# Kernel optimization log

Hardware: AMD Instinct MI355X
Metric: run time of the kernel (lower is better)

The kernel has to match this reference:

```python
import jax, jax.numpy as jnp
import numpy as np

B, S, H, NH, L = 2, 2048, 2048, 16, 512
HD = H // NH  # head_dim = 128


def setup_inputs() -> dict:
    key = jax.random.key(0)
    k1, k2, k3, k4, k5 = jax.random.split(key, 5)
    scale = 0.02  # mimic xavier-scale init
    return {
        "q": jax.random.normal(k1, (B, S, H), dtype=jnp.float32),
        "latent_kv": jax.random.normal(k2, (B, S, L), dtype=jnp.float32),
        "Wq": jax.random.normal(k3, (H, H), dtype=jnp.float32) * scale,
        "Wkv_expand": jax.random.normal(k4, (2 * H, L), dtype=jnp.float32) * scale,
        "Wout": jax.random.normal(k5, (H, H), dtype=jnp.float32) * scale,
    }


def reference(q, latent_kv, Wq, Wkv_expand, Wout):
    b, sq, _ = q.shape
    sk = latent_kv.shape[1]
    # projections (torch Linear: x @ W.T)
    qp = q @ Wq.T                              # [B,Sq,H]
    kv = latent_kv @ Wkv_expand.T              # [B,Sk,2H]
    k, v = jnp.split(kv, 2, axis=-1)           # each [B,Sk,H]
    # split heads -> [B,NH,S,HD]
    qh = qp.reshape(b, sq, NH, HD).transpose(0, 2, 1, 3)
    kh = k.reshape(b, sk, NH, HD).transpose(0, 2, 1, 3)
    vh = v.reshape(b, sk, NH, HD).transpose(0, 2, 1, 3)
    inv_sqrt_d = 1.0 / jnp.sqrt(jnp.float32(HD))
    scores = jnp.einsum("bhqd,bhkd->bhqk", qh, kh) * inv_sqrt_d
    # causal mask (seq_q == seq_k)
    causal = jnp.tril(jnp.ones((sq, sk), dtype=bool))
    scores = jnp.where(causal, scores, jnp.finfo(scores.dtype).min)
    attn = jax.nn.softmax(scores, axis=-1)
    out = jnp.einsum("bhqk,bhkd->bhqd", attn, vh)  # [B,NH,Sq,HD]
    out = out.transpose(0, 2, 1, 3).reshape(b, sq, H)
    return out @ Wout.T
```

## Files before the change

kernel.cpp:

```cpp
#include <hip/hip_runtime.h>

#define SLEN 2048
#define NHEADS 16
#define HDIM 128

typedef __attribute__((ext_vector_type(8))) short bf16x8;
typedef __attribute__((ext_vector_type(4))) float f32x4;
typedef __attribute__((ext_vector_type(16))) float f32x16;

__device__ __forceinline__ unsigned short f2bf(float f) {
  union { float f; unsigned u; } v; v.f = f;
  unsigned r = v.u + 0x7FFFu + ((v.u >> 16) & 1u);
  return (unsigned short)(r >> 16);
}

__device__ __forceinline__ float bf2f(unsigned short h) {
  union { unsigned u; float f; } v; v.u = (unsigned)h << 16;
  return v.f;
}

__device__ __forceinline__ unsigned pkbf(float a, float b) {
  unsigned r;
  asm("v_cvt_pk_bf16_f32 %0, %1, %2" : "=v"(r) : "v"(a), "v"(b));
  return r;
}

__device__ __forceinline__ void gload16(const void* g, void* l) {
  __builtin_amdgcn_global_load_lds(
      (const __attribute__((address_space(1))) unsigned int*)g,
      (__attribute__((address_space(3))) unsigned int*)l, 16, 0, 0);
}

__global__ __launch_bounds__(256) void cvt_all(const float* __restrict__ q,
                                               const float* __restrict__ Wq,
                                               const float* __restrict__ lat,
                                               const float* __restrict__ Wkv,
                                               const float* __restrict__ Wout,
                                               unsigned short* __restrict__ qo,
                                               unsigned short* __restrict__ Wqo,
                                               unsigned short* __restrict__ lato,
                                               unsigned short* __restrict__ Wkvo,
                                               unsigned short* __restrict__ Wouto) {
  const int blk = blockIdx.x;
  const float* in;
  unsigned short* out;
  int base;
  if (blk < 4096)      { in = q;    out = qo;    base = 0; }
  else if (blk < 6144) { in = Wq;   out = Wqo;   base = 4096; }
  else if (blk < 7168) { in = lat;  out = lato;  base = 6144; }
  else if (blk < 8192) { in = Wkv;  out = Wkvo;  base = 7168; }
  else                 { in = Wout; out = Wouto; base = 8192; }
  const int i = (blk - base) * 256 + threadIdx.x;
  const float4* p = reinterpret_cast<const float4*>(in) + (size_t)i * 2;
  float4 a = p[0], b = p[1];
  uint4 o;
  o.x = (unsigned)f2bf(a.x) | ((unsigned)f2bf(a.y) << 16);
  o.y = (unsigned)f2bf(a.z) | ((unsigned)f2bf(a.w) << 16);
  o.z = (unsigned)f2bf(b.x) | ((unsigned)f2bf(b.y) << 16);
  o.w = (unsigned)f2bf(b.z) | ((unsigned)f2bf(b.w) << 16);
  reinterpret_cast<uint4*>(out)[i] = o;
}

template <bool OUT_F32>
__global__ __launch_bounds__(256, 2) void gemm_bt(const unsigned short* __restrict__ A,
                                                  const unsigned short* __restrict__ B,
                                                  void* __restrict__ Cv,
                                                  int M, int N, int K,
                                                  size_t zB, size_t zC, float scale) {
  __shared__ unsigned short As[4][128 * 32];
  __shared__ unsigned short Bs[4][128 * 32];
  const int tid = threadIdx.x;
  const int lane = tid & 63, wid = tid >> 6;
  const int g = lane >> 4, q = lane & 15;
  const int nbx = N >> 7;
  const int cpx = gridDim.x >> 3;
  const int bid = (blockIdx.x & 7) * cpx + (blockIdx.x >> 3);
  const int bx = bid % nbx, by = bid / nbx;
  const int tM = by << 7, tN = bx << 7;
  const int wm = (wid >> 1) * 64, wn = (wid & 1) * 64;
  const size_t zoff = (size_t)blockIdx.z;
  B += zoff * zB;

  const int sr = tid >> 2, sc = tid & 3;
  const int scs = sc ^ (sr & 3);
  const unsigned short* gA0 = A + (size_t)(tM + sr) * K + (scs << 3);
  const unsigned short* gA1 = A + (size_t)(tM + 64 + sr) * K + (scs << 3);
  const unsigned short* gB0 = B + (size_t)(tN + sr) * K + (scs << 3);
  const unsigned short* gB1 = B + (size_t)(tN + 64 + sr) * K + (scs << 3);

  const int nk = K >> 5;
  const int gq = g ^ (q & 3);

  auto STAGE = [&](int slot, int kt) {
    const size_t ko = (size_t)kt << 5;
    unsigned short* ad = &As[slot][0] + tid * 8;
    unsigned short* bd = &Bs[slot][0] + tid * 8;
    gload16(gA0 + ko, ad);
    gload16(gA1 + ko, ad + 2048);
    gload16(gB0 + ko, bd);
    gload16(gB1 + ko, bd + 2048);
  };

  STAGE(0, 0); STAGE(1, 1); STAGE(2, 2);

  f32x4 acc[4][4] = {};

  for (int t = 0; t < nk; ++t) {
    if (t + 2 < nk)      asm volatile("s_waitcnt vmcnt(8)" ::: "memory");
    else if (t + 1 < nk) asm volatile("s_waitcnt vmcnt(4)" ::: "memory");
    else                 asm volatile("s_waitcnt vmcnt(0)" ::: "memory");
    __builtin_amdgcn_s_barrier();
    if (t + 3 < nk) STAGE((t + 3) & 3, t + 3);

    const int s = t & 3;
    bf16x8 af[4], bfr[4];
#pragma unroll
    for (int i = 0; i < 4; ++i)
      af[i] = *(const bf16x8*)&As[s][(wm + i * 16 + q) * 32 + gq * 8];
#pragma unroll
    for (int j = 0; j < 4; ++j)
      bfr[j] = *(const bf16x8*)&Bs[s][(wn + j * 16 + q) * 32 + gq * 8];
    __builtin_amdgcn_s_setprio(1);
#pragma unroll
    for (int i = 0; i < 4; ++i)
#pragma unroll
      for (int j = 0; j < 4; ++j)
        acc[i][j] = __builtin_amdgcn_mfma_f32_16x16x32_bf16(af[i], bfr[j], acc[i][j], 0, 0, 0);
    __builtin_amdgcn_s_setprio(0);
  }

  if constexpr (OUT_F32) {
    float* C = (float*)Cv + zoff * zC;
#pragma unroll
    for (int i = 0; i < 4; ++i)
#pragma unroll
      for (int j = 0; j < 4; ++j)
#pragma unroll
        for (int r = 0; r < 4; ++r)
          C[(size_t)(tM + wm + i * 16 + g * 4 + r) * N + (tN + wn + j * 16 + q)] =
              acc[i][j][r] * scale;
  } else {
    unsigned short* C = (unsigned short*)Cv + zoff * zC;
#pragma unroll
    for (int i = 0; i < 4; ++i)
#pragma unroll
      for (int j = 0; j < 4; ++j)
#pragma unroll
        for (int r = 0; r < 4; ++r)
          C[(size_t)(tM + wm + i * 16 + g * 4 + r) * N + (tN + wn + j * 16 + q)] =
              f2bf(acc[i][j][r] * scale);
  }
}

__global__ __launch_bounds__(256, 3) void mla_attn(const unsigned short* __restrict__ Q,
                                                   const unsigned short* __restrict__ K,
                                                   const unsigned short* __restrict__ VT,
                                                   unsigned short* __restrict__ Op0,
                                                   unsigned short* __restrict__ Op1,
                                                   float* __restrict__ Stats) {
  __shared__ unsigned short Ks[2][64 * 128];
  __shared__ unsigned short Vs[128 * 64];

  const int tid = threadIdx.x, lane = tid & 63, w = tid >> 6;
  const int q5 = lane & 31, half = lane >> 5, q7 = lane & 7;
  const int bh = blockIdx.x / 24;
  const int rem = blockIdx.x - bh * 24;
  const int pr = rem / 3, s3 = rem - pr * 3;
  const int head = bh & 15, b = bh >> 4;

  const unsigned short* Kbase = K + (size_t)(b * 2048) * 2048 + head * 128;
  const unsigned short* Vbase = VT + (size_t)(b * 2048 + head * 128) * 2048;

  const int r0 = tid >> 4, c0 = tid & 15;
  const unsigned short* kS = Kbase + (size_t)r0 * 2048 + ((c0 ^ r0) << 3);
  const int d0 = tid >> 3, c3 = tid & 7;
  const unsigned short* vS = Vbase + (size_t)d0 * 2048 + ((c3 ^ (d0 & 7)) << 3);

  const int arow0 = q5 * 256;
  const int vrow0 = q5 * 128;
  const int q15 = q5 & 15;

  for (int t2 = 0; t2 < 2; ++t2) {
    const int qt = t2 ? pr : 15 - pr;
    const int T = 2 * (qt + 1);
    const int kt0 = (T * s3) / 3;
    const int ktN = (T * (s3 + 1)) / 3;
    const int myq = qt * 128 + w * 32 + q5;
    const unsigned short* Qrow = Q + (size_t)(b * 2048 + myq) * 2048 + head * 128;

    bf16x8 qf[8];
#pragma unroll
    for (int ks = 0; ks < 8; ++ks)
      qf[ks] = *(const bf16x8*)((const char*)Qrow + ks * 32 + half * 16);

    __syncthreads();

    {
      unsigned short* kd = &Ks[kt0 & 1][0] + tid * 8;
      const unsigned short* ks2 = kS + (size_t)(kt0 * 64) * 2048;
#pragma unroll
      for (int u = 0; u < 4; ++u) gload16(ks2 + (size_t)u * 16 * 2048, kd + u * 2048);
    }

    float m2 = -1e30f, l = 0.f;
    f32x16 o[4];
#pragma unroll
    for (int i = 0; i < 16; ++i) { o[0][i] = 0.f; o[1][i] = 0.f; o[2][i] = 0.f; o[3][i] = 0.f; }

    for (int kt = kt0; kt < ktN; ++kt) {
      const int cur = kt & 1;
      asm volatile("s_waitcnt vmcnt(0)" ::: "memory");
      __builtin_amdgcn_s_barrier();

      {
        unsigned short* vd = &Vs[0] + tid * 8;
        const unsigned short* vs2 = vS + kt * 64;
#pragma unroll
        for (int u = 0; u < 4; ++u) gload16(vs2 + (size_t)u * 32 * 2048, vd + u * 2048);
      }
      if (kt + 1 < ktN) {
        unsigned short* kd = &Ks[cur ^ 1][0] + tid * 8;
        const unsigned short* ks2 = kS + (size_t)((kt + 1) * 64) * 2048;
#pragma unroll
        for (int u = 0; u < 4; ++u) gload16(ks2 + (size_t)u * 16 * 2048, kd + u * 2048);
      }

      f32x16 st[2];
#pragma unroll
      for (int i = 0; i < 16; ++i) { st[0][i] = 0.f; st[1][i] = 0.f; }
      const char* kb = (const char*)&Ks[cur][0];
      __builtin_amdgcn_s_setprio(1);
#pragma unroll
      for (int ks = 0; ks < 8; ++ks) {
        const int cd = ks * 2 + half;
#pragma unroll
        for (int m = 0; m < 2; ++m) {
          bf16x8 kf = *(const bf16x8*)(kb + arow0 + m * 8192 + ((cd ^ q15) << 4));
          st[m] = __builtin_amdgcn_mfma_f32_32x32x16_bf16(kf, qf[ks], st[m], 0, 0, 0);
        }
      }
      __builtin_amdgcn_s_setprio(0);

      float t[32];
      const int kvb = kt * 64;
      const bool needmask = (kvb + 63 > qt * 128 + w * 32);
#pragma unroll
      for (int m = 0; m < 2; ++m)
#pragma unroll
        for (int r = 0; r < 16; ++r) {
          float sv = st[m][r];
          if (needmask) {
            const int kvloc = m * 32 + (r & 3) + 8 * (r >> 2) + 4 * half;
            sv = (kvb + kvloc <= myq) ? sv : -3e38f;
          }
          t[m * 16 + r] = sv;
        }
      float mx = fmaxf(t[0], t[1]);
#pragma unroll
      for (int i = 2; i < 32; i += 2) mx = fmaxf(fmaxf(mx, t[i]), t[i + 1]);
      mx = fmaxf(mx, __shfl_xor(mx, 32));

      if (!__all(mx <= m2 + 11.54f)) {
        const float mnew = fmaxf(m2, mx);
        const float rsc = __builtin_amdgcn_exp2f(m2 - mnew);
        m2 = mnew; l *= rsc;
#pragma unroll
        for (int r = 0; r < 16; ++r) {
          const int rowv = (r & 3) + 8 * (r >> 2) + 4 * half;
          const float f = __shfl(rsc, rowv);
          o[0][r] *= f; o[1][r] *= f; o[2][r] *= f; o[3][r] *= f;
        }
      }

      float ts = 0.f;
#pragma unroll
      for (int i = 0; i < 32; ++i) { t[i] = __builtin_amdgcn_exp2f(t[i] - m2); ts += t[i]; }
      ts += __shfl_xor(ts, 32);
      l += ts;

      unsigned wpk[2][4][2];
#pragma unroll
      for (int m = 0; m < 2; ++m)
#pragma unroll
        for (int r4 = 0; r4 < 4; ++r4) {
          wpk[m][r4][0] = pkbf(t[m * 16 + r4 * 4 + 0], t[m * 16 + r4 * 4 + 1]);
          wpk[m][r4][1] = pkbf(t[m * 16 + r4 * 4 + 2], t[m * 16 + r4 * 4 + 3]);
        }

      if (kt + 1 < ktN) asm volatile("s_waitcnt vmcnt(4)" ::: "memory");
      else              asm volatile("s_waitcnt vmcnt(0)" ::: "memory");
      __builtin_amdgcn_s_barrier();

      const char* vb = (const char*)&Vs[0];
#pragma unroll
      for (int ks = 0; ks < 4; ++ks) {
        const int m = ks >> 1, i = ks & 1;
        const unsigned s0 = half ? wpk[m][2 * i][0] : wpk[m][2 * i + 1][0];
        const unsigned s1 = half ? wpk[m][2 * i][1] : wpk[m][2 * i + 1][1];
        const unsigned rv0 = (unsigned)__shfl_xor((int)s0, 32);
        const unsigned rv1 = (unsigned)__shfl_xor((int)s1, 32);
        const unsigned ow0 = half ? wpk[m][2 * i + 1][0] : wpk[m][2 * i][0];
        const unsigned ow1 = half ? wpk[m][2 * i + 1][1] : wpk[m][2 * i][1];
        union { unsigned u[4]; bf16x8 v; } fr;
        fr.u[0] = half ? rv0 : ow0;
        fr.u[1] = half ? rv1 : ow1;
        fr.u[2] = half ? ow0 : rv0;
        fr.u[3] = half ? ow1 : rv1;
        const int cd = ks * 2 + half;
        __builtin_amdgcn_s_setprio(1);
#pragma unroll
        for (int nf = 0; nf < 4; ++nf) {
          bf16x8 vf = *(const bf16x8*)(vb + vrow0 + nf * 4096 + ((cd ^ q7) << 4));
          o[nf] = __builtin_amdgcn_mfma_f32_32x32x16_bf16(fr.v, vf, o[nf], 0, 0, 0);
        }
        __builtin_amdgcn_s_setprio(0);
      }
    }

    const int set = (bh * 16 + qt) * 3 + s3;
    unsigned short* ob = (set < 1024) ? Op0 + ((size_t)set << 14)
                                      : Op1 + ((size_t)(set - 1024) << 14);
    if (half == 0) {
      Stats[(set << 8) + (w * 32 + q5) * 2] = m2;
      Stats[(set << 8) + (w * 32 + q5) * 2 + 1] = l;
    }
#pragma unroll
    for (int r = 0; r < 16; ++r) {
      const int rowv = (r & 3) + 8 * (r >> 2) + 4 * half;
      const int row = w * 32 + rowv;
#pragma unroll
      for (int nf = 0; nf < 4; ++nf)
        ob[row * 128 + nf * 32 + q5] = f2bf(o[nf][r]);
    }
  }
}

__global__ __launch_bounds__(256) void mla_merge(const unsigned short* __restrict__ Op0,
                                                 const unsigned short* __restrict__ Op1,
                                                 const float* __restrict__ St,
                                                 unsigned short* __restrict__ AO) {
  const int idx = blockIdx.x * 256 + threadIdx.x;
  const int rid = idx >> 4;
  const int d0 = (idx & 15) << 3;
  const int bhqt = rid >> 7;
  const int row = rid & 127;
  const int sb = bhqt * 3;
  float m[3], lv[3];
#pragma unroll
  for (int s = 0; s < 3; ++s) {
    m[s] = St[((sb + s) << 8) + row * 2];
    lv[s] = St[((sb + s) << 8) + row * 2 + 1];
  }
  const float M = fmaxf(fmaxf(m[0], m[1]), m[2]);
  float wgt[3], den = 0.f;
#pragma unroll
  for (int s = 0; s < 3; ++s) { wgt[s] = __builtin_amdgcn_exp2f(m[s] - M); den += wgt[s] * lv[s]; }
  const float inv = 1.0f / den;
  bf16x8 pa[3];
#pragma unroll
  for (int s = 0; s < 3; ++s) {
    const int set = sb + s;
    const unsigned short* p = (set < 1024) ? Op0 + ((size_t)set << 14)
                                           : Op1 + ((size_t)(set - 1024) << 14);
    pa[s] = *(const bf16x8*)(p + row * 128 + d0);
  }
  const int bh = bhqt >> 4, qt = bhqt & 15;
  const int head = bh & 15, b = bh >> 4;
  unsigned short outv[8];
#pragma unroll
  for (int j = 0; j < 8; ++j) {
    float acc = 0.f;
#pragma unroll
    for (int s = 0; s < 3; ++s) acc += wgt[s] * bf2f((unsigned short)pa[s][j]);
    outv[j] = f2bf(acc * inv);
  }
  unsigned short* dst = AO + ((size_t)(b * 2048 + qt * 128 + row)) * 2048 + head * 128 + d0;
  *(uint4*)dst = *(const uint4*)outv;
}

extern "C" void kernel_launch(void* const* d_in, const int* in_sizes, int n_in,
                              void* d_out, int out_size, void* d_ws, size_t ws_size,
                              hipStream_t stream) {
  const float* q    = (const float*)d_in[0];
  const float* lat  = (const float*)d_in[1];
  const float* Wq   = (const float*)d_in[2];
  const float* Wkv  = (const float*)d_in[3];
  const float* Wout = (const float*)d_in[4];

  char* ws = (char*)d_ws;
  unsigned short* qbf   = (unsigned short*)(ws);
  unsigned short* Op0   = (unsigned short*)(ws);
  unsigned short* Wqbf  = (unsigned short*)(ws + 16777216);
  unsigned short* latbf = (unsigned short*)(ws + 25165824);
  unsigned short* Wkvbf = (unsigned short*)(ws + 29360128);
  unsigned short* Wobf  = (unsigned short*)(ws + 33554432);
  unsigned short* qpbf  = (unsigned short*)(ws + 41943040);
  unsigned short* Kbf   = (unsigned short*)(ws + 58720256);
  unsigned short* aobf  = (unsigned short*)(ws + 58720256);
  unsigned short* VTbf  = (unsigned short*)(ws + 75497472);
  unsigned short* Wvbf  = Wkvbf + (size_t)2048 * 512;
  unsigned short* Op1   = (unsigned short*)d_out;
  float*          Stats = (float*)((char*)d_out + 16777216);

  const float SCALE_L2E = 0.12751742f;

  cvt_all<<<10240, 256, 0, stream>>>(q, Wq, lat, Wkv, Wout,
                                     qbf, Wqbf, latbf, Wkvbf, Wobf);

  gemm_bt<false><<<512, 256, 0, stream>>>(qbf, Wqbf, qpbf, 4096, 2048, 2048, 0, 0, SCALE_L2E);
  gemm_bt<false><<<512, 256, 0, stream>>>(latbf, Wkvbf, Kbf, 4096, 2048, 512, 0, 0, 1.0f);
  gemm_bt<false><<<dim3(256, 1, 2), 256, 0, stream>>>(
      Wvbf, latbf, VTbf, 2048, 2048, 512,
      (size_t)2048 * 512, (size_t)2048 * 2048, 1.0f);
  mla_attn<<<768, 256, 0, stream>>>(qpbf, Kbf, VTbf, Op0, Op1, Stats);
  mla_merge<<<4096, 256, 0, stream>>>(Op0, Op1, Stats, aobf);
  gemm_bt<true><<<512, 256, 0, stream>>>(aobf, Wobf, (float*)d_out, 4096, 2048, 2048, 0, 0, 1.0f);
}
```

Baseline: 237.9 us.

## Use 512-thread attention blocks with 256-row query tiles and double-buffered V

Restructures the attention kernel to use 8 waves per block covering 256 query rows, with the key range split into 4 equal chunks instead of 3. V tiles are now double-buffered alongside K so both are prefetched together, and the wait only requires the older loads to finish. The merge kernel and the partial-output and stats layouts are updated to match. Wout conversion moves to a separate kernel launched after attention so its buffer can reuse the freed VT space. This increases K/V reuse per block but raises LDS and register pressure and changes load balance across the causal tiles.

After: 320.1 us. 1.35x slower.

```diff
diff --git a/kernel.cpp b/kernel.cpp
--- a/kernel.cpp
+++ b/kernel.cpp
@@ -35,12 +35,10 @@
                                                const float* __restrict__ Wq,
                                                const float* __restrict__ lat,
                                                const float* __restrict__ Wkv,
-                                               const float* __restrict__ Wout,
                                                unsigned short* __restrict__ qo,
                                                unsigned short* __restrict__ Wqo,
                                                unsigned short* __restrict__ lato,
-                                               unsigned short* __restrict__ Wkvo,
-                                               unsigned short* __restrict__ Wouto) {
+                                               unsigned short* __restrict__ Wkvo) {
   const int blk = blockIdx.x;
   const float* in;
   unsigned short* out;
@@ -48,9 +46,21 @@
   if (blk < 4096)      { in = q;    out = qo;    base = 0; }
   else if (blk < 6144) { in = Wq;   out = Wqo;   base = 4096; }
   else if (blk < 7168) { in = lat;  out = lato;  base = 6144; }
-  else if (blk < 8192) { in = Wkv;  out = Wkvo;  base = 7168; }
-  else                 { in = Wout; out = Wouto; base = 8192; }
+  else                 { in = Wkv;  out = Wkvo;  base = 7168; }
   const int i = (blk - base) * 256 + threadIdx.x;
+  const float4* p = reinterpret_cast<const float4*>(in) + (size_t)i * 2;
+  float4 a = p[0], b = p[1];
+  uint4 o;
+  o.x = (unsigned)f2bf(a.x) | ((unsigned)f2bf(a.y) << 16);
+  o.y = (unsigned)f2bf(a.z) | ((unsigned)f2bf(a.w) << 16);
+  o.z = (unsigned)f2bf(b.x) | ((unsigned)f2bf(b.y) << 16);
+  o.w = (unsigned)f2bf(b.z) | ((unsigned)f2bf(b.w) << 16);
+  reinterpret_cast<uint4*>(out)[i] = o;
+}
+
+__global__ __launch_bounds__(256) void cvt_w(const float* __restrict__ in,
+                                             unsigned short* __restrict__ out) {
+  const int i = blockIdx.x * 256 + threadIdx.x;
   const float4* p = reinterpret_cast<const float4*>(in) + (size_t)i * 2;
   float4 a = p[0], b = p[1];
   uint4 o;
@@ -152,27 +162,27 @@
   }
 }
 
-__global__ __launch_bounds__(256, 3) void mla_attn(const unsigned short* __restrict__ Q,
+__global__ __launch_bounds__(512, 4) void mla_attn(const unsigned short* __restrict__ Q,
                                                    const unsigned short* __restrict__ K,
                                                    const unsigned short* __restrict__ VT,
                                                    unsigned short* __restrict__ Op0,
                                                    unsigned short* __restrict__ Op1,
                                                    float* __restrict__ Stats) {
   __shared__ unsigned short Ks[2][64 * 128];
-  __shared__ unsigned short Vs[128 * 64];
+  __shared__ unsigned short Vs[2][128 * 64];
 
   const int tid = threadIdx.x, lane = tid & 63, w = tid >> 6;
   const int q5 = lane & 31, half = lane >> 5, q7 = lane & 7;
-  const int bh = blockIdx.x / 24;
-  const int rem = blockIdx.x - bh * 24;
-  const int pr = rem / 3, s3 = rem - pr * 3;
+  const int s4 = blockIdx.x & 3;
+  const int pr = (blockIdx.x >> 2) & 3;
+  const int bh = blockIdx.x >> 4;
   const int head = bh & 15, b = bh >> 4;
 
   const unsigned short* Kbase = K + (size_t)(b * 2048) * 2048 + head * 128;
   const unsigned short* Vbase = VT + (size_t)(b * 2048 + head * 128) * 2048;
 
   const int r0 = tid >> 4, c0 = tid & 15;
-  const unsigned short* kS = Kbase + (size_t)r0 * 2048 + ((c0 ^ r0) << 3);
+  const unsigned short* kS = Kbase + (size_t)r0 * 2048 + ((c0 ^ (r0 & 15)) << 3);
   const int d0 = tid >> 3, c3 = tid & 7;
   const unsigned short* vS = Vbase + (size_t)d0 * 2048 + ((c3 ^ (d0 & 7)) << 3);
 
@@ -181,11 +191,10 @@
   const int q15 = q5 & 15;
 
   for (int t2 = 0; t2 < 2; ++t2) {
-    const int qt = t2 ? pr : 15 - pr;
-    const int T = 2 * (qt + 1);
-    const int kt0 = (T * s3) / 3;
-    const int ktN = (T * (s3 + 1)) / 3;
-    const int myq = qt * 128 + w * 32 + q5;
+    const int qt = t2 ? pr : 7 - pr;
+    const int kt0 = (qt + 1) * s4;
+    const int ktN = (qt + 1) * (s4 + 1);
+    const int myq = qt * 256 + w * 32 + q5;
     const unsigned short* Qrow = Q + (size_t)(b * 2048 + myq) * 2048 + head * 128;
 
     bf16x8 qf[8];
@@ -197,9 +206,13 @@
 
     {
       unsigned short* kd = &Ks[kt0 & 1][0] + tid * 8;
+      unsigned short* vd = &Vs[kt0 & 1][0] + tid * 8;
       const unsigned short* ks2 = kS + (size_t)(kt0 * 64) * 2048;
-#pragma unroll
-      for (int u = 0; u < 4; ++u) gload16(ks2 + (size_t)u * 16 * 2048, kd + u * 2048);
+      const unsigned short* vs2 = vS + kt0 * 64;
+      gload16(ks2, kd);
+      gload16(ks2 + (size_t)32 * 2048, kd + 4096);
+      gload16(vs2, vd);
+      gload16(vs2 + (size_t)64 * 2048, vd + 4096);
     }
 
     float m2 = -1e30f, l = 0.f;
@@ -209,20 +222,18 @@
 
     for (int kt = kt0; kt < ktN; ++kt) {
       const int cur = kt & 1;
-      asm volatile("s_waitcnt vmcnt(0)" ::: "memory");
+      asm volatile("s_waitcnt vmcnt(2)" ::: "memory");
       __builtin_amdgcn_s_barrier();
 
-      {
-        unsigned short* vd = &Vs[0] + tid * 8;
-        const unsigned short* vs2 = vS + kt * 64;
-#pragma unroll
-        for (int u = 0; u < 4; ++u) gload16(vs2 + (size_t)u * 32 * 2048, vd + u * 2048);
-      }
       if (kt + 1 < ktN) {
         unsigned short* kd = &Ks[cur ^ 1][0] + tid * 8;
+        unsigned short* vd = &Vs[cur ^ 1][0] + tid * 8;
         const unsigned short* ks2 = kS + (size_t)((kt + 1) * 64) * 2048;
-#pragma unroll
-        for (int u = 0; u < 4; ++u) gload16(ks2 + (size_t)u * 16 * 2048, kd + u * 2048);
+        const unsigned short* vs2 = vS + (kt + 1) * 64;
+        gload16(ks2, kd);
+        gload16(ks2 + (size_t)32 * 2048, kd + 4096);
+        gload16(vs2, vd);
+        gload16(vs2 + (size_t)64 * 2048, vd + 4096);
       }
 
       f32x16 st[2];
@@ -243,7 +254,7 @@
 
       float t[32];
       const int kvb = kt * 64;
-      const bool needmask = (kvb + 63 > qt * 128 + w * 32);
+      const bool needmask = (kvb + 63 > qt * 256 + w * 32);
 #pragma unroll
       for (int m = 0; m < 2; ++m)
 #pragma unroll
@@ -291,7 +302,7 @@
       else              asm volatile("s_waitcnt vmcnt(0)" ::: "memory");
       __builtin_amdgcn_s_barrier();
 
-      const char* vb = (const char*)&Vs[0];
+      const char* vb = (const char*)&Vs[cur][0];
 #pragma unroll
       for (int ks = 0; ks < 4; ++ks) {
         const int m = ks >> 1, i = ks & 1;
@@ -317,12 +328,12 @@
       }
     }
 
-    const int set = (bh * 16 + qt) * 3 + s3;
-    unsigned short* ob = (set < 1024) ? Op0 + ((size_t)set << 14)
-                                      : Op1 + ((size_t)(set - 1024) << 14);
+    const int set = (bh * 8 + qt) * 4 + s4;
+    unsigned short* ob = (set < 512) ? Op0 + ((size_t)set << 15)
+                                     : Op1 + ((size_t)(set - 512) << 15);
     if (half == 0) {
-      Stats[(set << 8) + (w * 32 + q5) * 2] = m2;
-      Stats[(set << 8) + (w * 32 + q5) * 2 + 1] = l;
+      Stats[(set << 9) + (w * 32 + q5) * 2] = m2;
+      Stats[(set << 9) + (w * 32 + q5) * 2 + 1] = l;
     }
 #pragma unroll
     for (int r = 0; r < 16; ++r) {
@@ -342,39 +353,39 @@
   const int idx = blockIdx.x * 256 + threadIdx.x;
   const int rid = idx >> 4;
   const int d0 = (idx & 15) << 3;
-  const int bhqt = rid >> 7;
-  const int row = rid & 127;
-  const int sb = bhqt * 3;
-  float m[3], lv[3];
-#pragma unroll
-  for (int s = 0; s < 3; ++s) {
-    m[s] = St[((sb + s) << 8) + row * 2];
-    lv[s] = St[((sb + s) << 8) + row * 2 + 1];
-  }
-  const float M = fmaxf(fmaxf(m[0], m[1]), m[2]);
-  float wgt[3], den = 0.f;
-#pragma unroll
-  for (int s = 0; s < 3; ++s) { wgt[s] = __builtin_amdgcn_exp2f(m[s] - M); den += wgt[s] * lv[s]; }
+  const int bhqt = rid >> 8;
+  const int row = rid & 255;
+  const int sb = bhqt << 2;
+  float m[4], lv[4];
+#pragma unroll
+  for (int s = 0; s < 4; ++s) {
+    m[s] = St[((sb + s) << 9) + row * 2];
+    lv[s] = St[((sb + s) << 9) + row * 2 + 1];
+  }
+  const float M = fmaxf(fmaxf(m[0], m[1]), fmaxf(m[2], m[3]));
+  float wgt[4], den = 0.f;
+#pragma unroll
+  for (int s = 0; s < 4; ++s) { wgt[s] = __builtin_amdgcn_exp2f(m[s] - M); den += wgt[s] * lv[s]; }
   const float inv = 1.0f / den;
-  bf16x8 pa[3];
-#pragma unroll
-  for (int s = 0; s < 3; ++s) {
+  bf16x8 pa[4];
+#pragma unroll
+  for (int s = 0; s < 4; ++s) {
     const int set = sb + s;
-    const unsigned short* p = (set < 1024) ? Op0 + ((size_t)set << 14)
-                                           : Op1 + ((size_t)(set - 1024) << 14);
+    const unsigned short* p = (set < 512) ? Op0 + ((size_t)set << 15)
+                                          : Op1 + ((size_t)(set - 512) << 15);
     pa[s] = *(const bf16x8*)(p + row * 128 + d0);
   }
-  const int bh = bhqt >> 4, qt = bhqt & 15;
+  const int bh = bhqt >> 3, qt = bhqt & 7;
   const int head = bh & 15, b = bh >> 4;
   unsigned short outv[8];
 #pragma unroll
   for (int j = 0; j < 8; ++j) {
     float acc = 0.f;
 #pragma unroll
-    for (int s = 0; s < 3; ++s) acc += wgt[s] * bf2f((unsigned short)pa[s][j]);
+    for (int s = 0; s < 4; ++s) acc += wgt[s] * bf2f((unsigned short)pa[s][j]);
     outv[j] = f2bf(acc * inv);
   }
-  unsigned short* dst = AO + ((size_t)(b * 2048 + qt * 128 + row)) * 2048 + head * 128 + d0;
+  unsigned short* dst = AO + ((size_t)(b * 2048 + qt * 256 + row)) * 2048 + head * 128 + d0;
   *(uint4*)dst = *(const uint4*)outv;
 }
 
@@ -393,26 +404,26 @@
   unsigned short* Wqbf  = (unsigned short*)(ws + 16777216);
   unsigned short* latbf = (unsigned short*)(ws + 25165824);
   unsigned short* Wkvbf = (unsigned short*)(ws + 29360128);
-  unsigned short* Wobf  = (unsigned short*)(ws + 33554432);
+  float*          Stats = (float*)(ws + 33554432);
   unsigned short* qpbf  = (unsigned short*)(ws + 41943040);
   unsigned short* Kbf   = (unsigned short*)(ws + 58720256);
   unsigned short* aobf  = (unsigned short*)(ws + 58720256);
   unsigned short* VTbf  = (unsigned short*)(ws + 75497472);
+  unsigned short* Wobf  = (unsigned short*)(ws + 75497472);
   unsigned short* Wvbf  = Wkvbf + (size_t)2048 * 512;
   unsigned short* Op1   = (unsigned short*)d_out;
-  float*          Stats = (float*)((char*)d_out + 16777216);
 
   const float SCALE_L2E = 0.12751742f;
 
-  cvt_all<<<10240, 256, 0, stream>>>(q, Wq, lat, Wkv, Wout,
-                                     qbf, Wqbf, latbf, Wkvbf, Wobf);
+  cvt_all<<<8192, 256, 0, stream>>>(q, Wq, lat, Wkv, qbf, Wqbf, latbf, Wkvbf);
 
   gemm_bt<false><<<512, 256, 0, stream>>>(qbf, Wqbf, qpbf, 4096, 2048, 2048, 0, 0, SCALE_L2E);
   gemm_bt<false><<<512, 256, 0, stream>>>(latbf, Wkvbf, Kbf, 4096, 2048, 512, 0, 0, 1.0f);
   gemm_bt<false><<<dim3(256, 1, 2), 256, 0, stream>>>(
       Wvbf, latbf, VTbf, 2048, 2048, 512,
       (size_t)2048 * 512, (size_t)2048 * 2048, 1.0f);
-  mla_attn<<<768, 256, 0, stream>>>(qpbf, Kbf, VTbf, Op0, Op1, Stats);
+  mla_attn<<<512, 512, 0, stream>>>(qpbf, Kbf, VTbf, Op0, Op1, Stats);
+  cvt_w<<<2048, 256, 0, stream>>>(Wout, Wobf);
   mla_merge<<<4096, 256, 0, stream>>>(Op0, Op1, Stats, aobf);
   gemm_bt<true><<<512, 256, 0, stream>>>(aobf, Wobf, (float*)d_out, 4096, 2048, 2048, 0, 0, 1.0f);
 }
```
